# Kernel tuning notes

Hardware: AMD Instinct MI355X
Metric: run time of the kernel (lower is better)

Reference implementation:

```python
import jax, jax.numpy as jnp
import numpy as np

BN_EPS = 1e-5


def setup_inputs() -> dict:
    key = jax.random.key(0)
    ks = jax.random.split(key, 8)
    B, C, T, H, W = 8, 64, 16, 56, 56
    Cr = C // 4  # ratio=4 bottleneck in RouteFuncMLP
    s = lambda k, shape, scale=0.05: jax.random.normal(k, shape, jnp.float32) * scale
    return {
        "x": jax.random.normal(ks[0], (B, C, T, H, W), jnp.float32),
        "view": 3,  # View.FOUL
        "emb": s(ks[1], (4, C), 1.0),
        "Wg": s(ks[2], (C, C)),
        "bg": jnp.zeros((C,), jnp.float32),
        "Wa": s(ks[3], (Cr, C, 3)),
        "ba": jnp.zeros((Cr,), jnp.float32),
        "bn_gamma": jnp.ones((Cr,), jnp.float32),
        "bn_beta": jnp.zeros((Cr,), jnp.float32),
        "bn_mean": jnp.zeros((Cr,), jnp.float32),
        "bn_var": jnp.ones((Cr,), jnp.float32),
        "Wb": s(ks[4], (C, Cr, 3)),
        "Wconv": s(ks[5], (C, C, 3, 3)),
        "Wcls": s(ks[6], (10, C)),
        "bcls": jnp.zeros((10,), jnp.float32),
    }


def _conv1d_t(x, w, pad):
    # Temporal conv: x [B, Cin, T], w [Cout, Cin, K] -> [B, Cout, T]
    return jax.lax.conv_general_dilated(
        x, w, window_strides=(1,), padding=[(pad, pad)],
        dimension_numbers=("NCH", "OIH", "NCH"))


def _route_func(x, Wg, bg, Wa, ba, bn_gamma, bn_beta, bn_mean, bn_var, Wb):
    # RouteFuncMLP: per-frame, per-channel calibration factors. x: [B,C,T,H,W]
    g = x.mean(axis=(2, 3, 4))  # global pool -> [B,C]
    xt = x.mean(axis=(3, 4))    # spatial pool -> [B,C,T]
    g = jnp.einsum("oc,bc->bo", Wg, g) + bg  # 1x1x1 conv on global branch
    h = _conv1d_t(xt + g[:, :, None], Wa, pad=1) + ba[None, :, None]  # [B,Cr,T]
    # BatchNorm3d (inference form with running stats)
    h = (h - bn_mean[None, :, None]) * jax.lax.rsqrt(bn_var[None, :, None] + BN_EPS)
    h = h * bn_gamma[None, :, None] + bn_beta[None, :, None]
    h = jax.nn.relu(h)
    return _conv1d_t(h, Wb, pad=1) + 1.0  # alpha: [B,C,T]


def reference(x, view, emb, Wg, bg, Wa, ba, bn_gamma, bn_beta, bn_mean, bn_var, Wb, Wconv, Wcls, bcls):
    B, C, T, H, W = x.shape
    # embed-add: broadcast the view embedding over T,H,W
    x = x + emb[view][None, :, None, None, None]
    alpha = _route_func(x, Wg, bg, Wa, ba, bn_gamma, bn_beta, bn_mean, bn_var, Wb)
    # TAdaConv2d with cal_dim='cin': scaling the shared kernel per input channel
    # (per batch, per frame) is mathematically identical to scaling the input
    # channels first and convolving with the shared kernel.
    xs = x * alpha[:, :, :, None, None]
    xs = xs.transpose(0, 2, 1, 3, 4).reshape(B * T, C, H, W)
    y = jax.lax.conv_general_dilated(
        xs, Wconv, window_strides=(1, 1), padding=[(1, 1), (1, 1)],
        dimension_numbers=("NCHW", "OIHW", "NCHW"))
    y = y.reshape(B, T, C, H, W).transpose(0, 2, 1, 3, 4)  # [B,C,T,H,W]
    pooled = y.max(axis=(2, 3, 4))  # max over T,H,W -> [B,C]
    return pooled @ Wcls.T + bcls   # [B,10]
```

## Files before the change

### kernel.cpp

```cpp
#include <hip/hip_runtime.h>
#include <math.h>

#define B_ 8
#define C_ 64
#define T_ 16
#define H_ 56
#define W_ 56
#define HW_ (H_ * W_)
#define CR_ 16
#define PLANE (T_ * HW_)

typedef __attribute__((ext_vector_type(8))) short bf16x8;
typedef __attribute__((ext_vector_type(4))) float f32x4;

__device__ __forceinline__ unsigned short f2bf(float f) {
    unsigned u = __float_as_uint(f);
    u += 0x7fffu + ((u >> 16) & 1u);
    return (unsigned short)(u >> 16);
}

__global__ __launch_bounds__(128) void pool_prepack_kernel(
    const float* __restrict__ x, const float* __restrict__ Wconv,
    float* __restrict__ xt, unsigned short* __restrict__ packWbf)
{
    int blk = blockIdx.x;
    int tid = threadIdx.x;
    if (blk >= 8192) {
        int idx = (blk - 8192) * 128 + tid;
        if (idx < 64 * 576) {
            int j     = idx & 7;
            int lane  = (idx >> 3) & 63;
            int mt    = (idx >> 9) & 3;
            int kstep = idx >> 11;
            int cih = kstep & 1, tap = kstep >> 1;
            int co = mt * 16 + (lane & 15);
            int ci = cih * 32 + (lane >> 4) * 8 + j;
            packWbf[idx] = f2bf(Wconv[(co * C_ + ci) * 9 + tap]);
        }
        return;
    }
    __shared__ float red[2];
    const float4* p = (const float4*)(x + (size_t)blk * HW_);
    float s = 0.f;
    #pragma unroll
    for (int k = 0; k < 7; ++k) {
        int i = tid + k * 128;
        if (i < 784) { float4 v = p[i]; s += (v.x + v.y) + (v.z + v.w); }
    }
    #pragma unroll
    for (int off = 32; off > 0; off >>= 1) s += __shfl_down(s, off);
    if ((tid & 63) == 0) red[tid >> 6] = s;
    __syncthreads();
    if (tid == 0) xt[blk] = red[0] + red[1];
}

#define LCOLS2 58
#define HROWE (4 * LCOLS2)

__global__ __launch_bounds__(256) void conv_mfma_kernel(
    const float* __restrict__ x, const float* __restrict__ emb,
    const int* __restrict__ viewp, const float* __restrict__ xt,
    const float* __restrict__ Wg, const float* __restrict__ bg,
    const float* __restrict__ Wa, const float* __restrict__ ba,
    const float* __restrict__ bng, const float* __restrict__ bnb,
    const float* __restrict__ bnm, const float* __restrict__ bnv,
    const float* __restrict__ Wb,
    const unsigned short* __restrict__ packWbf, float* __restrict__ part)
{
    __shared__ bf16x8 ltile[10 * HROWE];
    __shared__ float sa[C_], sea[C_];
    __shared__ float smax[4][C_];

    int blk = blockIdx.x;
    int strip = blk % 7;
    int bt = blk / 7;
    int b = bt >> 4, t = bt & 15;
    int h0 = strip * 8;
    int tid = threadIdx.x;
    int lane = tid & 63, wv = tid >> 6;
    int q4 = lane >> 4, li = lane & 15;

    float* scr = (float*)ltile;
    float* z   = scr;
    float* swa = scr + 1152;
    float* hsv = scr + 4288;
    float* ggv = scr + 4352;
    float* gsv = scr + 4416;

    {
        int view = viewp[0];
        for (int i = tid; i < 1024; i += 256) {
            int c = i >> 4, tt = i & 15;
            z[c * 18 + tt + 1] = xt[b * 1024 + i] * (1.f / HW_) + emb[view * C_ + c];
        }
        if (tid < 128) { int c = tid & 63; z[c * 18 + (tid < 64 ? 0 : 17)] = 0.f; }
        for (int i = tid; i < 3072; i += 256) {
            float v = Wa[i];
            int r = i / 192, rem = i - r * 192;
            int ii = rem / 3, tap = rem - ii * 3;
            swa[ii * 49 + r * 3 + tap] = v;
        }
    }
    __syncthreads();
    if (tid < 64) {
        float s = 0.f;
        #pragma unroll
        for (int k = 1; k <= 16; ++k) s += z[tid * 18 + k];
        gsv[tid] = s * (1.f / 16.f);
    }
    __syncthreads();
    {
        float p = 0.f;
        const float* wrow = Wg + tid * 16;
        int q = tid & 3;
        #pragma unroll
        for (int k = 0; k < 16; ++k) p = fmaf(wrow[k], gsv[q * 16 + k], p);
        p += __shfl_xor(p, 1);
        p += __shfl_xor(p, 2);
        if (q == 0) ggv[tid >> 2] = p + bg[tid >> 2];
    }
    __syncthreads();
    for (int i = tid; i < 1024; i += 256) {
        int c = i >> 4, tt = i & 15;
        z[c * 18 + tt + 1] += ggv[c];
    }
    __syncthreads();
    if (tid < 48) {
        int r = tid & 15, s = tid >> 4;
        int tp = t - 1 + s;
        float hv = 0.f;
        if ((unsigned)tp < 16u) {
            float v = ba[r];
            #pragma unroll 8
            for (int i2 = 0; i2 < 64; ++i2) {
                const float* wa = swa + i2 * 49 + r * 3;
                const float* zr = z + i2 * 18 + tp;
                v = fmaf(zr[0], wa[0], v);
                v = fmaf(zr[1], wa[1], v);
                v = fmaf(zr[2], wa[2], v);
            }
            v = (v - bnm[r]) * rsqrtf(bnv[r] + 1e-5f);
            v = fmaf(v, bng[r], bnb[r]);
            hv = fmaxf(v, 0.f);
        }
        hsv[r * 3 + s] = hv;
    }
    __syncthreads();
    {
        float p = 0.f;
        const float* wrow = Wb + tid * 12;
        int q = tid & 3;
        #pragma unroll
        for (int k = 0; k < 12; ++k) p = fmaf(wrow[k], hsv[q * 12 + k], p);
        p += __shfl_xor(p, 1);
        p += __shfl_xor(p, 2);
        if (q == 0) {
            int c = tid >> 2;
            float a = p + 1.f;
            sa[c] = a;
            sea[c] = emb[viewp[0] * C_ + c] * a;
        }
    }
    __syncthreads();

    if (tid >= 64 && tid < 144) {
        int i = tid - 64;
        int r = i / 8, c8 = i - r * 8;
        int ch4 = c8 >> 1, col = (c8 & 1) ? 57 : 0;
        ltile[(r * 4 + ch4) * LCOLS2 + col] = (bf16x8){0,0,0,0,0,0,0,0};
    }

    const float* xb = x + ((size_t)(b * C_) * T_ + t) * HW_;

    int baddr[7];
    #pragma unroll
    for (int nt = 0; nt < 7; ++nt) {
        int p = (wv * 7 + nt) * 16 + li;
        int row = p / W_, col = p - row * W_;
        baddr[nt] = row * HROWE + q4 * LCOLS2 + col;
    }

    f32x4 acc[7][4];
    #pragma unroll
    for (int nt = 0; nt < 7; ++nt)
        #pragma unroll
        for (int mt = 0; mt < 4; ++mt)
            acc[nt][mt] = (f32x4){0.f, 0.f, 0.f, 0.f};

    const bf16x8* pw = (const bf16x8*)packWbf;

    #pragma unroll
    for (int half = 0; half < 2; ++half) {
        __syncthreads();
        #pragma unroll
        for (int k = 0; k < 3; ++k) {
            int item = tid + k * 256;
            if (item < 560) {
                int ch4 = item / 140;
                int rem = item - ch4 * 140;
                int row = rem / 14, cq = rem - row * 14;
                int gr = h0 - 1 + row;
                int ci0 = half * 32 + ch4 * 8;
                bf16x8 hv[4] = {(bf16x8){0,0,0,0,0,0,0,0}, (bf16x8){0,0,0,0,0,0,0,0},
                                (bf16x8){0,0,0,0,0,0,0,0}, (bf16x8){0,0,0,0,0,0,0,0}};
                if ((unsigned)gr < (unsigned)H_) {
                    const float* src = xb + (size_t)ci0 * PLANE + gr * W_ + cq * 4;
                    float4 f[8];
                    #pragma unroll
                    for (int j = 0; j < 8; ++j)
                        f[j] = *(const float4*)(src + (size_t)j * PLANE);
                    #pragma unroll
                    for (int j = 0; j < 8; ++j) {
                        float aj = sa[ci0 + j], ej = sea[ci0 + j];
                        hv[0][j] = (short)f2bf(fmaf(f[j].x, aj, ej));
                        hv[1][j] = (short)f2bf(fmaf(f[j].y, aj, ej));
                        hv[2][j] = (short)f2bf(fmaf(f[j].z, aj, ej));
                        hv[3][j] = (short)f2bf(fmaf(f[j].w, aj, ej));
                    }
                }
                bf16x8* dst = &ltile[(row * 4 + ch4) * LCOLS2 + cq * 4 + 1];
                #pragma unroll
                for (int cc = 0; cc < 4; ++cc) dst[cc] = hv[cc];
            }
        }
        __syncthreads();

        #pragma unroll
        for (int tap = 0; tap < 9; ++tap) {
            const int kh = tap / 3, kw = tap % 3;
            const int kstep = tap * 2 + half;
            const int boff = kh * HROWE + kw;
            bf16x8 af[4];
            #pragma unroll
            for (int mt = 0; mt < 4; ++mt)
                af[mt] = pw[(kstep * 4 + mt) * 64 + lane];
            #pragma unroll
            for (int nt = 0; nt < 7; ++nt) {
                bf16x8 bfr = ltile[baddr[nt] + boff];
                #pragma unroll
                for (int mt = 0; mt < 4; ++mt)
                    acc[nt][mt] = __builtin_amdgcn_mfma_f32_16x16x32_bf16(
                        af[mt], bfr, acc[nt][mt], 0, 0, 0);
            }
        }
    }

    float m[4][4];
    #pragma unroll
    for (int mt = 0; mt < 4; ++mt)
        #pragma unroll
        for (int i = 0; i < 4; ++i) {
            float v = acc[0][mt][i];
            #pragma unroll
            for (int nt = 1; nt < 7; ++nt) v = fmaxf(v, acc[nt][mt][i]);
            m[mt][i] = v;
        }
    #pragma unroll
    for (int off = 1; off < 16; off <<= 1)
        #pragma unroll
        for (int mt = 0; mt < 4; ++mt)
            #pragma unroll
            for (int i = 0; i < 4; ++i)
                m[mt][i] = fmaxf(m[mt][i], __shfl_xor(m[mt][i], off));
    if (li == 0) {
        #pragma unroll
        for (int mt = 0; mt < 4; ++mt)
            #pragma unroll
            for (int i = 0; i < 4; ++i)
                smax[wv][mt * 16 + q4 * 4 + i] = m[mt][i];
    }
    __syncthreads();
    if (tid < C_) {
        float mm = fmaxf(fmaxf(smax[0][tid], smax[1][tid]),
                         fmaxf(smax[2][tid], smax[3][tid]));
        part[(size_t)blk * C_ + tid] = mm;
    }
}

__global__ __launch_bounds__(512) void cls_kernel(
    const float* __restrict__ part, const float* __restrict__ Wcls,
    const float* __restrict__ bcls, float* __restrict__ out)
{
    __shared__ float pooled[512];
    int tid = threadIdx.x;
    int b = tid >> 6, c = tid & 63;
    const float* pb = part + (size_t)b * 112 * C_ + c;
    float m0 = -INFINITY, m1 = -INFINITY, m2 = -INFINITY, m3 = -INFINITY;
    #pragma unroll
    for (int i = 0; i < 28; ++i) {
        m0 = fmaxf(m0, pb[(i     ) * C_]);
        m1 = fmaxf(m1, pb[(i + 28) * C_]);
        m2 = fmaxf(m2, pb[(i + 56) * C_]);
        m3 = fmaxf(m3, pb[(i + 84) * C_]);
    }
    pooled[tid] = fmaxf(fmaxf(m0, m1), fmaxf(m2, m3));
    __syncthreads();
    if (tid < B_ * 10) {
        int bb = tid / 10, k = tid - (tid / 10) * 10;
        float v = bcls[k];
        #pragma unroll 8
        for (int cc = 0; cc < C_; ++cc)
            v = fmaf(pooled[bb * C_ + cc], Wcls[k * C_ + cc], v);
        out[tid] = v;
    }
}

extern "C" void kernel_launch(void* const* d_in, const int* in_sizes, int n_in,
                              void* d_out, int out_size, void* d_ws, size_t ws_size,
                              hipStream_t stream)
{
    const float* x     = (const float*)d_in[0];
    const int*   view  = (const int*)  d_in[1];
    const float* emb   = (const float*)d_in[2];
    const float* Wg    = (const float*)d_in[3];
    const float* bg    = (const float*)d_in[4];
    const float* Wa    = (const float*)d_in[5];
    const float* ba    = (const float*)d_in[6];
    const float* bng   = (const float*)d_in[7];
    const float* bnb   = (const float*)d_in[8];
    const float* bnm   = (const float*)d_in[9];
    const float* bnv   = (const float*)d_in[10];
    const float* Wb    = (const float*)d_in[11];
    const float* Wconv = (const float*)d_in[12];
    const float* Wcls  = (const float*)d_in[13];
    const float* bcls  = (const float*)d_in[14];
    float* out = (float*)d_out;

    char* wsb = (char*)d_ws;
    float*          xt      = (float*)(wsb + 0);
    float*          part    = (float*)(wsb + 32768);
    unsigned short* packWbf = (unsigned short*)(wsb + 262144);

    hipLaunchKernelGGL(pool_prepack_kernel, dim3(8192 + 288), dim3(128), 0, stream,
                       x, Wconv, xt, packWbf);
    hipLaunchKernelGGL(conv_mfma_kernel, dim3(B_ * T_ * 7), dim3(256), 0, stream,
                       x, emb, view, xt, Wg, bg, Wa, ba, bng, bnb, bnm, bnv, Wb,
                       packWbf, part);
    hipLaunchKernelGGL(cls_kernel, dim3(1), dim3(512), 0, stream,
                       part, Wcls, bcls, out);
}
```

Baseline: 82.52 us.

## Split conv output channels across 8 waves, swizzle LDS tile, remap blocks to XCDs

The conv kernel now runs 512 threads per block. Each group of four waves covers the same pixels, and the two groups split the 64 output channels in half, so each wave keeps half the accumulators and has more waves in flight. LDS tile addresses go through an XOR swizzle to reduce bank conflicts on the bf16x8 reads. Block indices are permuted so consecutive blocks spread across the 8 XCDs. The cost is a duplicated tile load per channel group, more barrier participants, and a strided staging loop that leaves most threads idle on the second pass.

```diff
diff --git a/kernel.cpp b/kernel.cpp
--- a/kernel.cpp
+++ b/kernel.cpp
@@ -18,6 +18,8 @@
     u += 0x7fffu + ((u >> 16) & 1u);
     return (unsigned short)(u >> 16);
 }
+
+__device__ __forceinline__ int swz(int m) { return m ^ ((m >> 3) & 7); }
 
 __global__ __launch_bounds__(128) void pool_prepack_kernel(
     const float* __restrict__ x, const float* __restrict__ Wconv,
@@ -57,7 +59,7 @@
 #define LCOLS2 58
 #define HROWE (4 * LCOLS2)
 
-__global__ __launch_bounds__(256) void conv_mfma_kernel(
+__global__ __launch_bounds__(512, 4) void conv_mfma_kernel(
     const float* __restrict__ x, const float* __restrict__ emb,
     const int* __restrict__ viewp, const float* __restrict__ xt,
     const float* __restrict__ Wg, const float* __restrict__ bg,
@@ -69,9 +71,10 @@
 {
     __shared__ bf16x8 ltile[10 * HROWE];
     __shared__ float sa[C_], sea[C_];
-    __shared__ float smax[4][C_];
-
-    int blk = blockIdx.x;
+    __shared__ float smax[8][C_];
+
+    int hw  = blockIdx.x;
+    int blk = (hw & 7) * 112 + (hw >> 3);
     int strip = blk % 7;
     int bt = blk / 7;
     int b = bt >> 4, t = bt & 15;
@@ -79,6 +82,7 @@
     int tid = threadIdx.x;
     int lane = tid & 63, wv = tid >> 6;
     int q4 = lane >> 4, li = lane & 15;
+    int g = wv & 3, mp = wv >> 2;
 
     float* scr = (float*)ltile;
     float* z   = scr;
@@ -89,12 +93,12 @@
 
     {
         int view = viewp[0];
-        for (int i = tid; i < 1024; i += 256) {
+        for (int i = tid; i < 1024; i += 512) {
             int c = i >> 4, tt = i & 15;
             z[c * 18 + tt + 1] = xt[b * 1024 + i] * (1.f / HW_) + emb[view * C_ + c];
         }
         if (tid < 128) { int c = tid & 63; z[c * 18 + (tid < 64 ? 0 : 17)] = 0.f; }
-        for (int i = tid; i < 3072; i += 256) {
+        for (int i = tid; i < 3072; i += 512) {
             float v = Wa[i];
             int r = i / 192, rem = i - r * 192;
             int ii = rem / 3, tap = rem - ii * 3;
@@ -109,7 +113,7 @@
         gsv[tid] = s * (1.f / 16.f);
     }
     __syncthreads();
-    {
+    if (tid < 256) {
         float p = 0.f;
         const float* wrow = Wg + tid * 16;
         int q = tid & 3;
@@ -120,7 +124,7 @@
         if (q == 0) ggv[tid >> 2] = p + bg[tid >> 2];
     }
     __syncthreads();
-    for (int i = tid; i < 1024; i += 256) {
+    for (int i = tid; i < 1024; i += 512) {
         int c = i >> 4, tt = i & 15;
         z[c * 18 + tt + 1] += ggv[c];
     }
@@ -146,7 +150,7 @@
         hsv[r * 3 + s] = hv;
     }
     __syncthreads();
-    {
+    if (tid < 256) {
         float p = 0.f;
         const float* wrow = Wb + tid * 12;
         int q = tid & 3;
@@ -167,7 +171,7 @@
         int i = tid - 64;
         int r = i / 8, c8 = i - r * 8;
         int ch4 = c8 >> 1, col = (c8 & 1) ? 57 : 0;
-        ltile[(r * 4 + ch4) * LCOLS2 + col] = (bf16x8){0,0,0,0,0,0,0,0};
+        ltile[swz((r * 4 + ch4) * LCOLS2 + col)] = (bf16x8){0,0,0,0,0,0,0,0};
     }
 
     const float* xb = x + ((size_t)(b * C_) * T_ + t) * HW_;
@@ -175,53 +179,54 @@
     int baddr[7];
     #pragma unroll
     for (int nt = 0; nt < 7; ++nt) {
-        int p = (wv * 7 + nt) * 16 + li;
+        int p = (g * 7 + nt) * 16 + li;
         int row = p / W_, col = p - row * W_;
         baddr[nt] = row * HROWE + q4 * LCOLS2 + col;
     }
 
-    f32x4 acc[7][4];
+    f32x4 acc[7][2];
     #pragma unroll
     for (int nt = 0; nt < 7; ++nt)
         #pragma unroll
-        for (int mt = 0; mt < 4; ++mt)
-            acc[nt][mt] = (f32x4){0.f, 0.f, 0.f, 0.f};
+        for (int mi = 0; mi < 2; ++mi)
+            acc[nt][mi] = (f32x4){0.f, 0.f, 0.f, 0.f};
 
     const bf16x8* pw = (const bf16x8*)packWbf;
 
     #pragma unroll
     for (int half = 0; half < 2; ++half) {
         __syncthreads();
-        #pragma unroll
-        for (int k = 0; k < 3; ++k) {
-            int item = tid + k * 256;
-            if (item < 560) {
-                int ch4 = item / 140;
-                int rem = item - ch4 * 140;
-                int row = rem / 14, cq = rem - row * 14;
-                int gr = h0 - 1 + row;
-                int ci0 = half * 32 + ch4 * 8;
-                bf16x8 hv[4] = {(bf16x8){0,0,0,0,0,0,0,0}, (bf16x8){0,0,0,0,0,0,0,0},
-                                (bf16x8){0,0,0,0,0,0,0,0}, (bf16x8){0,0,0,0,0,0,0,0}};
-                if ((unsigned)gr < (unsigned)H_) {
-                    const float* src = xb + (size_t)ci0 * PLANE + gr * W_ + cq * 4;
-                    float4 f[8];
+        for (int it = tid; it < 560; it += 512) {
+            int ch4 = it / 140;
+            int rem = it - ch4 * 140;
+            int row = rem / 14, cq = rem - row * 14;
+            int gr = h0 - 1 + row;
+            int ci0 = half * 32 + ch4 * 8;
+            bf16x8 hv[4] = {(bf16x8){0,0,0,0,0,0,0,0}, (bf16x8){0,0,0,0,0,0,0,0},
+                            (bf16x8){0,0,0,0,0,0,0,0}, (bf16x8){0,0,0,0,0,0,0,0}};
+            if ((unsigned)gr < (unsigned)H_) {
+                const float* src = xb + (size_t)ci0 * PLANE + gr * W_ + cq * 4;
+                #pragma unroll
+                for (int jb = 0; jb < 2; ++jb) {
+                    float4 f4[4];
                     #pragma unroll
-                    for (int j = 0; j < 8; ++j)
-                        f[j] = *(const float4*)(src + (size_t)j * PLANE);
+                    for (int j = 0; j < 4; ++j)
+                        f4[j] = *(const float4*)(src + (size_t)(jb * 4 + j) * PLANE);
                     #pragma unroll
-                    for (int j = 0; j < 8; ++j) {
-                        float aj = sa[ci0 + j], ej = sea[ci0 + j];
-                        hv[0][j] = (short)f2bf(fmaf(f[j].x, aj, ej));
-                        hv[1][j] = (short)f2bf(fmaf(f[j].y, aj, ej));
-                        hv[2][j] = (short)f2bf(fmaf(f[j].z, aj, ej));
-                        hv[3][j] = (short)f2bf(fmaf(f[j].w, aj, ej));
+                    for (int j = 0; j < 4; ++j) {
+                        int jj = jb * 4 + j;
+                        float aj = sa[ci0 + jj], ej = sea[ci0 + jj];
+                        hv[0][jj] = (short)f2bf(fmaf(f4[j].x, aj, ej));
+                        hv[1][jj] = (short)f2bf(fmaf(f4[j].y, aj, ej));
+                        hv[2][jj] = (short)f2bf(fmaf(f4[j].z, aj, ej));
+                        hv[3][jj] = (short)f2bf(fmaf(f4[j].w, aj, ej));
                     }
                 }
-                bf16x8* dst = &ltile[(row * 4 + ch4) * LCOLS2 + cq * 4 + 1];
-                #pragma unroll
-                for (int cc = 0; cc < 4; ++cc) dst[cc] = hv[cc];
             }
+            int base = (row * 4 + ch4) * LCOLS2 + cq * 4 + 1;
+            #pragma unroll
+            for (int cc = 0; cc < 4; ++cc)
+                ltile[swz(base + cc)] = hv[cc];
         }
         __syncthreads();
 
@@ -230,49 +235,50 @@
             const int kh = tap / 3, kw = tap % 3;
             const int kstep = tap * 2 + half;
             const int boff = kh * HROWE + kw;
-            bf16x8 af[4];
-            #pragma unroll
-            for (int mt = 0; mt < 4; ++mt)
-                af[mt] = pw[(kstep * 4 + mt) * 64 + lane];
+            bf16x8 af[2];
+            #pragma unroll
+            for (int mi = 0; mi < 2; ++mi)
+                af[mi] = pw[(kstep * 4 + (mp * 2 + mi)) * 64 + lane];
             #pragma unroll
             for (int nt = 0; nt < 7; ++nt) {
-                bf16x8 bfr = ltile[baddr[nt] + boff];
+                bf16x8 bfr = ltile[swz(baddr[nt] + boff)];
                 #pragma unroll
-                for (int mt = 0; mt < 4; ++mt)
-                    acc[nt][mt] = __builtin_amdgcn_mfma_f32_16x16x32_bf16(
-                        af[mt], bfr, acc[nt][mt], 0, 0, 0);
+                for (int mi = 0; mi < 2; ++mi)
+                    acc[nt][mi] = __builtin_amdgcn_mfma_f32_16x16x32_bf16(
+                        af[mi], bfr, acc[nt][mi], 0, 0, 0);
             }
         }
     }
 
-    float m[4][4];
-    #pragma unroll
-    for (int mt = 0; mt < 4; ++mt)
+    float m[2][4];
+    #pragma unroll
+    for (int mi = 0; mi < 2; ++mi)
         #pragma unroll
         for (int i = 0; i < 4; ++i) {
-            float v = acc[0][mt][i];
-            #pragma unroll
-            for (int nt = 1; nt < 7; ++nt) v = fmaxf(v, acc[nt][mt][i]);
-            m[mt][i] = v;
+            float v = acc[0][mi][i];
+            #pragma unroll
+            for (int nt = 1; nt < 7; ++nt) v = fmaxf(v, acc[nt][mi][i]);
+            m[mi][i] = v;
         }
     #pragma unroll
     for (int off = 1; off < 16; off <<= 1)
         #pragma unroll
-        for (int mt = 0; mt < 4; ++mt)
+        for (int mi = 0; mi < 2; ++mi)
             #pragma unroll
             for (int i = 0; i < 4; ++i)
-                m[mt][i] = fmaxf(m[mt][i], __shfl_xor(m[mt][i], off));
+                m[mi][i] = fmaxf(m[mi][i], __shfl_xor(m[mi][i], off));
     if (li == 0) {
         #pragma unroll
-        for (int mt = 0; mt < 4; ++mt)
+        for (int mi = 0; mi < 2; ++mi)
             #pragma unroll
             for (int i = 0; i < 4; ++i)
-                smax[wv][mt * 16 + q4 * 4 + i] = m[mt][i];
+                smax[wv][(mp * 2 + mi) * 16 + q4 * 4 + i] = m[mi][i];
     }
     __syncthreads();
     if (tid < C_) {
-        float mm = fmaxf(fmaxf(smax[0][tid], smax[1][tid]),
-                         fmaxf(smax[2][tid], smax[3][tid]));
+        float mm = smax[0][tid];
+        #pragma unroll
+        for (int w = 1; w < 8; ++w) mm = fmaxf(mm, smax[w][tid]);
         part[(size_t)blk * C_ + tid] = mm;
     }
 }
@@ -333,7 +339,7 @@
 
     hipLaunchKernelGGL(pool_prepack_kernel, dim3(8192 + 288), dim3(128), 0, stream,
                        x, Wconv, xt, packWbf);
-    hipLaunchKernelGGL(conv_mfma_kernel, dim3(B_ * T_ * 7), dim3(256), 0, stream,
+    hipLaunchKernelGGL(conv_mfma_kernel, dim3(B_ * T_ * 7), dim3(512), 0, stream,
                        x, emb, view, xt, Wg, bg, Wa, ba, bng, bnb, bnm, bnv, Wb,
                        packWbf, part);
     hipLaunchKernelGGL(cls_kernel, dim3(1), dim3(512), 0, stream,
```

Measured after the change: 110.5 us. 34.0% more time.

## Prefetch input tiles into registers to overlap global loads with routing and MFMA

Applied to the files above, without the earlier changes.

Global loads of the first channel half are issued at kernel start, so they overlap the route-function MLP computation. The second half's loads are issued before the first half's MFMA loop, hiding their latency behind compute. This holds three 8-element float4 buffers (96 floats) per thread across the compute, which raises register pressure alongside the 112 accumulator floats and may cut occupancy or cause spills.

```diff
diff --git a/kernel.cpp b/kernel.cpp
--- a/kernel.cpp
+++ b/kernel.cpp
@@ -57,6 +57,45 @@
 #define LCOLS2 58
 #define HROWE (4 * LCOLS2)
 
+__device__ __forceinline__ void ld_item(const float* xb, int it, int half,
+                                        int h0, float4* f) {
+    int ch4 = it / 140;
+    int rem = it - ch4 * 140;
+    int row = rem / 14, cq = rem - row * 14;
+    int gr = h0 - 1 + row;
+    if ((unsigned)gr < (unsigned)H_) {
+        const float* src = xb + (size_t)(half * 32 + ch4 * 8) * PLANE + gr * W_ + cq * 4;
+        #pragma unroll
+        for (int j = 0; j < 8; ++j)
+            f[j] = *(const float4*)(src + (size_t)j * PLANE);
+    }
+}
+
+__device__ __forceinline__ void st_item(bf16x8* ltile, const float* sa,
+                                        const float* sea, int it, int half,
+                                        int h0, const float4* f) {
+    int ch4 = it / 140;
+    int rem = it - ch4 * 140;
+    int row = rem / 14, cq = rem - row * 14;
+    int gr = h0 - 1 + row;
+    int ci0 = half * 32 + ch4 * 8;
+    bf16x8 hv[4] = {(bf16x8){0,0,0,0,0,0,0,0}, (bf16x8){0,0,0,0,0,0,0,0},
+                    (bf16x8){0,0,0,0,0,0,0,0}, (bf16x8){0,0,0,0,0,0,0,0}};
+    if ((unsigned)gr < (unsigned)H_) {
+        #pragma unroll
+        for (int j = 0; j < 8; ++j) {
+            float aj = sa[ci0 + j], ej = sea[ci0 + j];
+            hv[0][j] = (short)f2bf(fmaf(f[j].x, aj, ej));
+            hv[1][j] = (short)f2bf(fmaf(f[j].y, aj, ej));
+            hv[2][j] = (short)f2bf(fmaf(f[j].z, aj, ej));
+            hv[3][j] = (short)f2bf(fmaf(f[j].w, aj, ej));
+        }
+    }
+    int base = (row * 4 + ch4) * LCOLS2 + cq * 4 + 1;
+    #pragma unroll
+    for (int cc = 0; cc < 4; ++cc) ltile[base + cc] = hv[cc];
+}
+
 __global__ __launch_bounds__(256) void conv_mfma_kernel(
     const float* __restrict__ x, const float* __restrict__ emb,
     const int* __restrict__ viewp, const float* __restrict__ xt,
@@ -79,6 +118,12 @@
     int tid = threadIdx.x;
     int lane = tid & 63, wv = tid >> 6;
     int q4 = lane >> 4, li = lane & 15;
+
+    const float* xb = x + ((size_t)(b * C_) * T_ + t) * HW_;
+    float4 fA[8], fB[8], fC[8];
+    ld_item(xb, tid, 0, h0, fA);
+    ld_item(xb, tid + 256, 0, h0, fB);
+    if (tid < 48) ld_item(xb, tid + 512, 0, h0, fC);
 
     float* scr = (float*)ltile;
     float* z   = scr;
@@ -170,7 +215,14 @@
         ltile[(r * 4 + ch4) * LCOLS2 + col] = (bf16x8){0,0,0,0,0,0,0,0};
     }
 
-    const float* xb = x + ((size_t)(b * C_) * T_ + t) * HW_;
+    st_item(ltile, sa, sea, tid, 0, h0, fA);
+    st_item(ltile, sa, sea, tid + 256, 0, h0, fB);
+    if (tid < 48) st_item(ltile, sa, sea, tid + 512, 0, h0, fC);
+    __syncthreads();
+
+    ld_item(xb, tid, 1, h0, fA);
+    ld_item(xb, tid + 256, 1, h0, fB);
+    if (tid < 48) ld_item(xb, tid + 512, 1, h0, fC);
 
     int baddr[7];
     #pragma unroll
@@ -190,58 +242,46 @@
     const bf16x8* pw = (const bf16x8*)packWbf;
 
     #pragma unroll
-    for (int half = 0; half < 2; ++half) {
-        __syncthreads();
-        #pragma unroll
-        for (int k = 0; k < 3; ++k) {
-            int item = tid + k * 256;
-            if (item < 560) {
-                int ch4 = item / 140;
-                int rem = item - ch4 * 140;
-                int row = rem / 14, cq = rem - row * 14;
-                int gr = h0 - 1 + row;
-                int ci0 = half * 32 + ch4 * 8;
-                bf16x8 hv[4] = {(bf16x8){0,0,0,0,0,0,0,0}, (bf16x8){0,0,0,0,0,0,0,0},
-                                (bf16x8){0,0,0,0,0,0,0,0}, (bf16x8){0,0,0,0,0,0,0,0}};
-                if ((unsigned)gr < (unsigned)H_) {
-                    const float* src = xb + (size_t)ci0 * PLANE + gr * W_ + cq * 4;
-                    float4 f[8];
-                    #pragma unroll
-                    for (int j = 0; j < 8; ++j)
-                        f[j] = *(const float4*)(src + (size_t)j * PLANE);
-                    #pragma unroll
-                    for (int j = 0; j < 8; ++j) {
-                        float aj = sa[ci0 + j], ej = sea[ci0 + j];
-                        hv[0][j] = (short)f2bf(fmaf(f[j].x, aj, ej));
-                        hv[1][j] = (short)f2bf(fmaf(f[j].y, aj, ej));
-                        hv[2][j] = (short)f2bf(fmaf(f[j].z, aj, ej));
-                        hv[3][j] = (short)f2bf(fmaf(f[j].w, aj, ej));
-                    }
-                }
-                bf16x8* dst = &ltile[(row * 4 + ch4) * LCOLS2 + cq * 4 + 1];
-                #pragma unroll
-                for (int cc = 0; cc < 4; ++cc) dst[cc] = hv[cc];
-            }
-        }
-        __syncthreads();
-
-        #pragma unroll
-        for (int tap = 0; tap < 9; ++tap) {
-            const int kh = tap / 3, kw = tap % 3;
-            const int kstep = tap * 2 + half;
-            const int boff = kh * HROWE + kw;
-            bf16x8 af[4];
+    for (int tap = 0; tap < 9; ++tap) {
+        const int kh = tap / 3, kw = tap % 3;
+        const int kstep = tap * 2;
+        const int boff = kh * HROWE + kw;
+        bf16x8 af[4];
+        #pragma unroll
+        for (int mt = 0; mt < 4; ++mt)
+            af[mt] = pw[(kstep * 4 + mt) * 64 + lane];
+        #pragma unroll
+        for (int nt = 0; nt < 7; ++nt) {
+            bf16x8 bfr = ltile[baddr[nt] + boff];
             #pragma unroll
             for (int mt = 0; mt < 4; ++mt)
-                af[mt] = pw[(kstep * 4 + mt) * 64 + lane];
-            #pragma unroll
-            for (int nt = 0; nt < 7; ++nt) {
-                bf16x8 bfr = ltile[baddr[nt] + boff];
-                #pragma unroll
-                for (int mt = 0; mt < 4; ++mt)
-                    acc[nt][mt] = __builtin_amdgcn_mfma_f32_16x16x32_bf16(
-                        af[mt], bfr, acc[nt][mt], 0, 0, 0);
-            }
+                acc[nt][mt] = __builtin_amdgcn_mfma_f32_16x16x32_bf16(
+                    af[mt], bfr, acc[nt][mt], 0, 0, 0);
+        }
+    }
+    __syncthreads();
+
+    st_item(ltile, sa, sea, tid, 1, h0, fA);
+    st_item(ltile, sa, sea, tid + 256, 1, h0, fB);
+    if (tid < 48) st_item(ltile, sa, sea, tid + 512, 1, h0, fC);
+    __syncthreads();
+
+    #pragma unroll
+    for (int tap = 0; tap < 9; ++tap) {
+        const int kh = tap / 3, kw = tap % 3;
+        const int kstep = tap * 2 + 1;
+        const int boff = kh * HROWE + kw;
+        bf16x8 af[4];
+        #pragma unroll
+        for (int mt = 0; mt < 4; ++mt)
+            af[mt] = pw[(kstep * 4 + mt) * 64 + lane];
+        #pragma unroll
+        for (int nt = 0; nt < 7; ++nt) {
+            bf16x8 bfr = ltile[baddr[nt] + boff];
+            #pragma unroll
+            for (int mt = 0; mt < 4; ++mt)
+                acc[nt][mt] = __builtin_amdgcn_mfma_f32_16x16x32_bf16(
+                    af[mt], bfr, acc[nt][mt], 0, 0, 0);
         }
     }
 
```

Measured after the change: 122.6 us. 48.6% more time.

## Stage conv input tiles via global_load_lds into an fp32 LDS buffer

Applied to the files above, without the earlier changes.

Replaces direct per-thread float4 global loads of the input halo with async global_load_lds DMA copies of contiguous row spans into a new fp32 LDS staging buffer. The staging runs in four channel groups per half, each followed by a conversion step where only 140 threads scale, convert to bf16 and write the MFMA tile. This aims for coalesced, register-free global transfers, but it adds about 17.5KB of LDS per block, which may reduce occupancy. It also adds many more barriers and serializes load and convert with no overlap.

```diff
diff --git a/kernel.cpp b/kernel.cpp
--- a/kernel.cpp
+++ b/kernel.cpp
@@ -17,6 +17,13 @@
     unsigned u = __float_as_uint(f);
     u += 0x7fffu + ((u >> 16) & 1u);
     return (unsigned short)(u >> 16);
+}
+
+__device__ __forceinline__ void gload_lds16(const void* g, void* l) {
+    __builtin_amdgcn_global_load_lds(
+        (const __attribute__((address_space(1))) unsigned int*)g,
+        (__attribute__((address_space(3))) unsigned int*)l,
+        16, 0, 0);
 }
 
 __global__ __launch_bounds__(128) void pool_prepack_kernel(
@@ -68,6 +75,7 @@
     const unsigned short* __restrict__ packWbf, float* __restrict__ part)
 {
     __shared__ bf16x8 ltile[10 * HROWE];
+    __shared__ float fbuf[8 * 560];
     __shared__ float sa[C_], sea[C_];
     __shared__ float smax[4][C_];
 
@@ -172,6 +180,11 @@
 
     const float* xb = x + ((size_t)(b * C_) * T_ + t) * HW_;
 
+    int row0   = (h0 == 0) ? 0 : h0 - 1;
+    int rend   = (h0 + 9 > 56) ? 56 : h0 + 9;
+    int bytes  = (rend - row0) * 224;
+    int ldsoff = (h0 == 0) ? 56 : 0;
+
     int baddr[7];
     #pragma unroll
     for (int nt = 0; nt < 7; ++nt) {
@@ -191,24 +204,31 @@
 
     #pragma unroll
     for (int half = 0; half < 2; ++half) {
-        __syncthreads();
-        #pragma unroll
-        for (int k = 0; k < 3; ++k) {
-            int item = tid + k * 256;
-            if (item < 560) {
-                int ch4 = item / 140;
-                int rem = item - ch4 * 140;
-                int row = rem / 14, cq = rem - row * 14;
-                int gr = h0 - 1 + row;
-                int ci0 = half * 32 + ch4 * 8;
+        for (int g = 0; g < 4; ++g) {
+            #pragma unroll
+            for (int pj = 0; pj < 2; ++pj) {
+                int j = wv * 2 + pj;
+                const char* src = (const char*)(xb +
+                    (size_t)(half * 32 + g * 8 + j) * PLANE + row0 * W_);
+                float* dst = fbuf + j * 560 + ldsoff;
+                #pragma unroll
+                for (int s = 0; s < 3; ++s) {
+                    if (lane * 16 + s * 1024 < bytes)
+                        gload_lds16(src + s * 1024 + lane * 16, dst + s * 256);
+                }
+            }
+            __syncthreads();
+            if (tid < 140) {
+                int row = tid / 14, cq = tid - row * 14;
+                bool valid = !((h0 == 0 && row == 0) || (h0 == 48 && row == 9));
+                int ci0 = half * 32 + g * 8;
                 bf16x8 hv[4] = {(bf16x8){0,0,0,0,0,0,0,0}, (bf16x8){0,0,0,0,0,0,0,0},
                                 (bf16x8){0,0,0,0,0,0,0,0}, (bf16x8){0,0,0,0,0,0,0,0}};
-                if ((unsigned)gr < (unsigned)H_) {
-                    const float* src = xb + (size_t)ci0 * PLANE + gr * W_ + cq * 4;
+                if (valid) {
                     float4 f[8];
                     #pragma unroll
                     for (int j = 0; j < 8; ++j)
-                        f[j] = *(const float4*)(src + (size_t)j * PLANE);
+                        f[j] = *(const float4*)&fbuf[j * 560 + row * 56 + cq * 4];
                     #pragma unroll
                     for (int j = 0; j < 8; ++j) {
                         float aj = sa[ci0 + j], ej = sea[ci0 + j];
@@ -218,12 +238,12 @@
                         hv[3][j] = (short)f2bf(fmaf(f[j].w, aj, ej));
                     }
                 }
-                bf16x8* dst = &ltile[(row * 4 + ch4) * LCOLS2 + cq * 4 + 1];
+                bf16x8* dst = &ltile[(row * 4 + g) * LCOLS2 + cq * 4 + 1];
                 #pragma unroll
                 for (int cc = 0; cc < 4; ++cc) dst[cc] = hv[cc];
             }
-        }
-        __syncthreads();
+            __syncthreads();
+        }
 
         #pragma unroll
         for (int tap = 0; tap < 9; ++tap) {
@@ -243,6 +263,7 @@
                         af[mt], bfr, acc[nt][mt], 0, 0, 0);
             }
         }
+        if (half == 0) __syncthreads();
     }
 
     float m[4][4];
```

Result: slower. 84.97 us (+3.0%).
